# Performance work log

Hardware: AMD Instinct MI355X
Metric: run time of the kernel (lower is better)

The kernel has to match this reference:

```python
import jax, jax.numpy as jnp
import numpy as np

B, S, H = 32, 4096, 512

def setup_inputs() -> dict:
    key = jax.random.key(0)
    k1, k2, k3 = jax.random.split(key, 3)
    enc_output = jax.random.normal(k1, (B, S, H), dtype=jnp.float32)
    dec_output = jax.random.normal(k2, (B, 1, H), dtype=jnp.float32)
    # nn.Linear(H, H, bias=False) weight, applied as x @ W.T
    W = jax.random.normal(k3, (H, H), dtype=jnp.float32) * (1.0 / np.sqrt(H))
    return {"enc_output": enc_output, "dec_output": dec_output, "W": W}

def reference(enc_output, dec_output, W):
    # query = linear(dec_output.squeeze(1))  -> [B, H]
    query = jnp.einsum('bh,oh->bo', dec_output[:, 0, :], W)
    # scores = bmm(enc_output, query[..., None]).squeeze(-1) -> [B, S]
    scores = jnp.einsum('bsh,bh->bs', enc_output, query)
    # NOTE: original stores softmax(scores) in self.weight but uses the
    # RAW (pre-softmax) scores for the context bmm; reproduced faithfully.
    # context = bmm(scores[:, None, :], enc_output) -> [B, 1, H]
    context = jnp.einsum('bs,bsh->bh', scores, enc_output)[:, None, :]
    return context
```

## Files before the change

kernel.cpp:

```cpp
#include <hip/hip_runtime.h>

#define BB 32
#define SS 4096
#define HH 512

__global__ __launch_bounds__(256) void query_kernel(const float* __restrict__ dec,
                                                    const float* __restrict__ W,
                                                    float* __restrict__ q) {
    const int gwave = (blockIdx.x * 256 + threadIdx.x) >> 6;
    const int lane  = threadIdx.x & 63;
    const int b = gwave >> 9;
    const int o = gwave & 511;

    const float4* wrow = (const float4*)(W  + (size_t)o * HH);
    const float4* drow = (const float4*)(dec + (size_t)b * HH);

    float4 w0 = wrow[lane], w1 = wrow[64 + lane];
    float4 d0 = drow[lane], d1 = drow[64 + lane];

    float s = w0.x*d0.x + w0.y*d0.y + w0.z*d0.z + w0.w*d0.w
            + w1.x*d1.x + w1.y*d1.y + w1.z*d1.z + w1.w*d1.w;

    #pragma unroll
    for (int off = 32; off >= 1; off >>= 1)
        s += __shfl_down(s, off, 64);

    if (lane == 0) q[gwave] = s;
}

__global__ __launch_bounds__(256) void fused_kernel(const float* __restrict__ enc,
                                                    const float* __restrict__ q,
                                                    float* __restrict__ out) {
    const int lane = threadIdx.x & 63;
    const int wave = threadIdx.x >> 6;
    const int b     = blockIdx.x >> 5;
    const int chunk = blockIdx.x & 31;

    const float4* q4 = (const float4*)(q + (size_t)b * HH);
    const float4 q0 = q4[lane];
    const float4 q1 = q4[64 + lane];

    float4 acc0 = {0.f, 0.f, 0.f, 0.f};
    float4 acc1 = {0.f, 0.f, 0.f, 0.f};

    const int rowBase = chunk * 128 + wave * 32;
    const float4* encBase = (const float4*)(enc + ((size_t)b * SS + rowBase) * HH);

    #pragma unroll 2
    for (int r = 0; r < 32; ++r) {
        const float4* erow = encBase + (size_t)r * 128;
        float4 e0 = erow[lane];
        float4 e1 = erow[64 + lane];

        float dot = e0.x*q0.x + e0.y*q0.y + e0.z*q0.z + e0.w*q0.w
                  + e1.x*q1.x + e1.y*q1.y + e1.z*q1.z + e1.w*q1.w;

        #pragma unroll
        for (int off = 1; off < 64; off <<= 1)
            dot += __shfl_xor(dot, off, 64);

        acc0.x += dot * e0.x; acc0.y += dot * e0.y;
        acc0.z += dot * e0.z; acc0.w += dot * e0.w;
        acc1.x += dot * e1.x; acc1.y += dot * e1.y;
        acc1.z += dot * e1.z; acc1.w += dot * e1.w;
    }

    __shared__ float cbuf[4][HH];
    float* cw = cbuf[wave];
    const int c0 = lane * 4;
    cw[c0 + 0] = acc0.x; cw[c0 + 1] = acc0.y; cw[c0 + 2] = acc0.z; cw[c0 + 3] = acc0.w;
    cw[256 + c0 + 0] = acc1.x; cw[256 + c0 + 1] = acc1.y;
    cw[256 + c0 + 2] = acc1.z; cw[256 + c0 + 3] = acc1.w;
    __syncthreads();

    for (int c = threadIdx.x; c < HH; c += 256) {
        float v = cbuf[0][c] + cbuf[1][c] + cbuf[2][c] + cbuf[3][c];
        atomicAdd(out + (size_t)b * HH + c, v);
    }
}

extern "C" void kernel_launch(void* const* d_in, const int* in_sizes, int n_in,
                              void* d_out, int out_size, void* d_ws, size_t ws_size,
                              hipStream_t stream) {
    const float* enc = (const float*)d_in[0];
    const float* dec = (const float*)d_in[1];
    const float* W   = (const float*)d_in[2];
    float* out = (float*)d_out;
    float* q   = (float*)d_ws;

    hipMemsetAsync(d_out, 0, (size_t)BB * HH * sizeof(float), stream);

    query_kernel<<<dim3(4096), dim3(256), 0, stream>>>(dec, W, q);

    fused_kernel<<<dim3(1024), dim3(256), 0, stream>>>(enc, q, out);
}
```

Baseline: 368.2 us.

## Batch four rows per iteration with nontemporal loads and double the grid

The fused kernel now loads four encoder rows at once with nontemporal loads and interleaves their shuffle reductions. This exposes more memory-level parallelism and hides the latency of the serial cross-lane reduction. The grid doubles to 2048 blocks, each covering 64 rows instead of 128, to raise occupancy. In exchange it uses more registers and issues twice as many atomic adds to the output.

Result: faster. 342.1 us (-7.1%).

```diff
diff --git a/kernel.cpp b/kernel.cpp
--- a/kernel.cpp
+++ b/kernel.cpp
@@ -3,6 +3,8 @@
 #define BB 32
 #define SS 4096
 #define HH 512
+
+typedef float f4 __attribute__((ext_vector_type(4)));
 
 __global__ __launch_bounds__(256) void query_kernel(const float* __restrict__ dec,
                                                     const float* __restrict__ W,
@@ -12,11 +14,11 @@
     const int b = gwave >> 9;
     const int o = gwave & 511;
 
-    const float4* wrow = (const float4*)(W  + (size_t)o * HH);
-    const float4* drow = (const float4*)(dec + (size_t)b * HH);
+    const f4* wrow = (const f4*)(W  + (size_t)o * HH);
+    const f4* drow = (const f4*)(dec + (size_t)b * HH);
 
-    float4 w0 = wrow[lane], w1 = wrow[64 + lane];
-    float4 d0 = drow[lane], d1 = drow[64 + lane];
+    f4 w0 = wrow[lane], w1 = wrow[64 + lane];
+    f4 d0 = drow[lane], d1 = drow[64 + lane];
 
     float s = w0.x*d0.x + w0.y*d0.y + w0.z*d0.z + w0.w*d0.w
             + w1.x*d1.x + w1.y*d1.y + w1.z*d1.z + w1.w*d1.w;
@@ -33,44 +35,54 @@
                                                     float* __restrict__ out) {
     const int lane = threadIdx.x & 63;
     const int wave = threadIdx.x >> 6;
-    const int b     = blockIdx.x >> 5;
-    const int chunk = blockIdx.x & 31;
+    const int b     = blockIdx.x >> 6;
+    const int chunk = blockIdx.x & 63;
 
-    const float4* q4 = (const float4*)(q + (size_t)b * HH);
-    const float4 q0 = q4[lane];
-    const float4 q1 = q4[64 + lane];
+    const f4* q4 = (const f4*)(q + (size_t)b * HH);
+    const f4 q0 = q4[lane];
+    const f4 q1 = q4[64 + lane];
 
-    float4 acc0 = {0.f, 0.f, 0.f, 0.f};
-    float4 acc1 = {0.f, 0.f, 0.f, 0.f};
+    f4 acc0 = {0.f, 0.f, 0.f, 0.f};
+    f4 acc1 = {0.f, 0.f, 0.f, 0.f};
 
-    const int rowBase = chunk * 128 + wave * 32;
-    const float4* encBase = (const float4*)(enc + ((size_t)b * SS + rowBase) * HH);
+    const int rowBase = chunk * 64 + wave * 16;
+    const f4* encBase = (const f4*)(enc + ((size_t)b * SS + rowBase) * HH);
 
-    #pragma unroll 2
-    for (int r = 0; r < 32; ++r) {
-        const float4* erow = encBase + (size_t)r * 128;
-        float4 e0 = erow[lane];
-        float4 e1 = erow[64 + lane];
+    for (int rb = 0; rb < 16; rb += 4) {
+        f4 e0[4], e1[4];
+        #pragma unroll
+        for (int r = 0; r < 4; ++r) {
+            const f4* erow = encBase + (size_t)(rb + r) * 128;
+            e0[r] = __builtin_nontemporal_load(erow + lane);
+            e1[r] = __builtin_nontemporal_load(erow + 64 + lane);
+        }
 
-        float dot = e0.x*q0.x + e0.y*q0.y + e0.z*q0.z + e0.w*q0.w
-                  + e1.x*q1.x + e1.y*q1.y + e1.z*q1.z + e1.w*q1.w;
+        float dot[4];
+        #pragma unroll
+        for (int r = 0; r < 4; ++r)
+            dot[r] = e0[r].x*q0.x + e0[r].y*q0.y + e0[r].z*q0.z + e0[r].w*q0.w
+                   + e1[r].x*q1.x + e1[r].y*q1.y + e1[r].z*q1.z + e1[r].w*q1.w;
 
         #pragma unroll
-        for (int off = 1; off < 64; off <<= 1)
-            dot += __shfl_xor(dot, off, 64);
+        for (int off = 1; off < 64; off <<= 1) {
+            #pragma unroll
+            for (int r = 0; r < 4; ++r)
+                dot[r] += __shfl_xor(dot[r], off, 64);
+        }
 
-        acc0.x += dot * e0.x; acc0.y += dot * e0.y;
-        acc0.z += dot * e0.z; acc0.w += dot * e0.w;
-        acc1.x += dot * e1.x; acc1.y += dot * e1.y;
-        acc1.z += dot * e1.z; acc1.w += dot * e1.w;
+        #pragma unroll
+        for (int r = 0; r < 4; ++r) {
+            acc0.x += dot[r] * e0[r].x; acc0.y += dot[r] * e0[r].y;
+            acc0.z += dot[r] * e0[r].z; acc0.w += dot[r] * e0[r].w;
+            acc1.x += dot[r] * e1[r].x; acc1.y += dot[r] * e1[r].y;
+            acc1.z += dot[r] * e1[r].z; acc1.w += dot[r] * e1[r].w;
+        }
     }
 
     __shared__ float cbuf[4][HH];
     float* cw = cbuf[wave];
-    const int c0 = lane * 4;
-    cw[c0 + 0] = acc0.x; cw[c0 + 1] = acc0.y; cw[c0 + 2] = acc0.z; cw[c0 + 3] = acc0.w;
-    cw[256 + c0 + 0] = acc1.x; cw[256 + c0 + 1] = acc1.y;
-    cw[256 + c0 + 2] = acc1.z; cw[256 + c0 + 3] = acc1.w;
+    ((f4*)(cw))[lane]       = acc0;
+    ((f4*)(cw + 256))[lane] = acc1;
     __syncthreads();
 
     for (int c = threadIdx.x; c < HH; c += 256) {
@@ -88,9 +100,9 @@
     float* out = (float*)d_out;
     float* q   = (float*)d_ws;
 
-    hipMemsetAsync(d_out, 0, (size_t)BB * HH * sizeof(float), stream);
+    (void)hipMemsetAsync(d_out, 0, (size_t)BB * HH * sizeof(float), stream);
 
     query_kernel<<<dim3(4096), dim3(256), 0, stream>>>(dec, W, q);
 
-    fused_kernel<<<dim3(1024), dim3(256), 0, stream>>>(enc, q, out);
+    fused_kernel<<<dim3(2048), dim3(256), 0, stream>>>(enc, q, out);
 }
```
